# Performance work log

Hardware: AMD Instinct MI355X
Metric: run time of the kernel (lower is better)

## Reference

```python
import jax, jax.numpy as jnp
import numpy as np

PS, PAD, STRIDE = 3, 1, 1  # patch_size, padding, strides


def _unfold(x, ps, pad, stride):
    # torch F.unfold: [N, C, H, W] -> [N, C*ps*ps, L], channel-major (c, i, j) ordering
    N, C, H, Wd = x.shape
    xp = jnp.pad(x, ((0, 0), (0, 0), (pad, pad), (pad, pad)))
    Ho = (H + 2 * pad - ps) // stride + 1
    Wo = (Wd + 2 * pad - ps) // stride + 1
    cols = [xp[:, :, i:i + stride * Ho:stride, j:j + stride * Wo:stride]
            for i in range(ps) for j in range(ps)]  # ps*ps tensors of [N, C, Ho, Wo]
    cols = jnp.stack(cols, axis=2)                  # [N, C, ps*ps, Ho, Wo]
    return cols.reshape(N, C * ps * ps, Ho * Wo)


def _fold(cols, out_hw, ps, pad, stride):
    # torch F.fold (scatter-add inverse of unfold)
    N, CPP, L = cols.shape
    C = CPP // (ps * ps)
    H, Wd = out_hw
    Ho = (H + 2 * pad - ps) // stride + 1
    Wo = (Wd + 2 * pad - ps) // stride + 1
    cols = cols.reshape(N, C, ps, ps, Ho, Wo)
    out = jnp.zeros((N, C, H + 2 * pad, Wd + 2 * pad), cols.dtype)
    for i in range(ps):
        for j in range(ps):
            out = out.at[:, :, i:i + stride * Ho:stride, j:j + stride * Wo:stride].add(cols[:, :, i, j])
    return out[:, :, pad:pad + H, pad:pad + Wd]


def _l2norm(x, eps=1e-12):
    n = jnp.sqrt(jnp.sum(x * x, axis=-1, keepdims=True))
    return x / jnp.maximum(n, eps)


def setup_inputs() -> dict:
    key = jax.random.key(0)
    k1, k2, k3, k4 = jax.random.split(key, 4)
    shp = (2, 64, 5, 5, 48, 48)  # b, c, ah, aw, h, w
    return {
        "x1": jax.random.normal(k1, shp, dtype=jnp.float32),
        "x2": jax.random.normal(k2, shp, dtype=jnp.float32),
        "x3": jax.random.normal(k3, shp, dtype=jnp.float32),
        "W": jax.random.normal(k4, (8, 64), dtype=jnp.float32) * 0.05,  # 1x1 conv, c -> c//8
    }


def reference(x1, x2, x3, W):
    b, c, ah, aw, h, w = x1.shape
    A = ah * aw

    def flat(x):  # b c ah aw h w -> (b ah aw) c h w
        return x.transpose(0, 2, 3, 1, 4, 5).reshape(b * A, c, h, w)

    q = jnp.einsum('oc,nchw->nohw', W, flat(x1))  # 1x1 conv, no bias
    k = jnp.einsum('oc,nchw->nohw', W, flat(x2))
    v = flat(x3)

    qc = _unfold(q, PS, PAD, STRIDE)  # [(b ah aw), p_q, L]
    kc = _unfold(k, PS, PAD, STRIDE)
    vc = _unfold(v, PS, PAD, STRIDE)  # [(b ah aw), p_v, L]
    L = vc.shape[-1]
    p_v = vc.shape[1]

    def re(t):  # (b ah aw) p n -> b n (ah aw p)
        p = t.shape[1]
        return t.reshape(b, A, p, L).transpose(0, 3, 1, 2).reshape(b, L, A * p)

    Q = _l2norm(re(qc))
    K = _l2norm(re(kc))
    V = re(vc)  # [b, L, A*p_v]

    attn = jnp.einsum('bnd,bmd->bnm', Q, K)       # [b, L, L] cosine similarity
    idx = jnp.argmax(attn, axis=-1)               # [b, L] hard attention
    out = jnp.take_along_axis(V, idx[:, :, None], axis=1)  # gather rows of V

    # b n (ah aw p) -> (b ah aw) p n
    out = out.reshape(b, L, A, p_v).transpose(0, 2, 3, 1).reshape(b * A, p_v, L)
    out = _fold(out, (h, w), PS, PAD, STRIDE)     # [(b ah aw), c, h, w]
    return out.reshape(b, ah, aw, c, h, w).transpose(0, 3, 1, 2, 4, 5)
```

## Files before the change

### kernel.cpp

```cpp
#include <hip/hip_runtime.h>
#include <math.h>
#include <float.h>

#define NPIX 2304
#define NPAD 2500
#define PLANE 573440
#define MARGIN 3e-4f

#define OFF_QP     0u
#define OFF_KP     1146880u
#define OFF_PLANES 2293760u
#define OFF_NK     4587520u
#define OFF_INVNK  4592520u
#define OFF_PVAL   4597128u
#define OFF_PSEC   4818312u
#define OFF_PIDX   5039496u
#define OFF_IDX    5260680u
#define OFF_S      5269896u
#define OFF_SOFF   OFF_S
#define SSTRIDE    6250000L
#define PLANE_SH   573440

typedef __attribute__((ext_vector_type(8))) short short8;
typedef __attribute__((ext_vector_type(4))) float f32x4;

__device__ __forceinline__ unsigned short bfhi(float f) {
    unsigned u = __float_as_uint(f);
    return (unsigned short)((u + 0x7FFFu + ((u >> 16) & 1u)) >> 16);
}

__device__ __forceinline__ void gload_lds16(const void* g, void* l) {
    __builtin_amdgcn_global_load_lds(
        (const __attribute__((address_space(1))) unsigned int*)g,
        (__attribute__((address_space(3))) unsigned int*)l, 16, 0, 0);
}

__global__ __launch_bounds__(256) void k_zero(float4* __restrict__ p, int n4) {
    int i = blockIdx.x * 256 + threadIdx.x;
    const int stride = gridDim.x * 256;
    const float4 z = { 0.f, 0.f, 0.f, 0.f };
    for (; i < n4; i += stride) p[i] = z;
}

__global__ __launch_bounds__(256) void k_qk(const float* __restrict__ x1,
                                            const float* __restrict__ x2,
                                            const float* __restrict__ W,
                                            float* __restrict__ qp,
                                            float* __restrict__ kp,
                                            unsigned short* __restrict__ planes) {
    __shared__ float Ws[512];
    const int t = threadIdx.x;
    Ws[t] = W[t];
    Ws[t + 256] = W[t + 256];
    __syncthreads();
    const int img = blockIdx.x / 9;
    const int chunk = blockIdx.x % 9;
    const int pix = chunk * 256 + t;
    const int b = img / 25, a = img % 25;
    const int y = pix / 48, x = pix % 48;

    float q[8], k[8];
#pragma unroll
    for (int o = 0; o < 8; ++o) { q[o] = 0.f; k[o] = 0.f; }

    const float* p1 = x1 + (size_t)b * 64 * 57600 + a * 2304 + pix;
    const float* p2 = x2 + (size_t)b * 64 * 57600 + a * 2304 + pix;
#pragma unroll 8
    for (int c = 0; c < 64; ++c) {
        float v1 = p1[c * 57600];
        float v2 = p2[c * 57600];
#pragma unroll
        for (int o = 0; o < 8; ++o) {
            float w = Ws[o * 64 + c];
            q[o] = fmaf(w, v1, q[o]);
            k[o] = fmaf(w, v2, k[o]);
        }
    }
    const int p = (y + 1) * 50 + (x + 1);
    float* qd = qp + (size_t)b * PLANE + (size_t)p * 224 + a * 8;
    float* kd = kp + (size_t)b * PLANE + (size_t)p * 224 + a * 8;
    float4 q0 = { q[0], q[1], q[2], q[3] }, q1 = { q[4], q[5], q[6], q[7] };
    float4 k0 = { k[0], k[1], k[2], k[3] }, k1 = { k[4], k[5], k[6], k[7] };
    *(float4*)qd = q0; *(float4*)(qd + 4) = q1;
    *(float4*)kd = k0; *(float4*)(kd + 4) = k1;

    const int P = p >> 7, r = p & 127, cc = a >> 2, dq = a & 3;
    const int g = r * 4 + ((dq + (r >> 1)) & 3);
    const size_t goff = ((size_t)(P * 7 + cc) * 512 + g) * 8;
    short8 qh, ql, kh, kl;
#pragma unroll
    for (int o = 0; o < 8; ++o) {
        unsigned short h = bfhi(q[o]);
        qh[o] = (short)h;
        ql[o] = (short)bfhi(q[o] - __uint_as_float(((unsigned)h) << 16));
        h = bfhi(k[o]);
        kh[o] = (short)h;
        kl[o] = (short)bfhi(k[o] - __uint_as_float(((unsigned)h) << 16));
    }
    *(short8*)(planes + (size_t)(0 * 2 + b) * PLANE_SH + goff) = qh;
    *(short8*)(planes + (size_t)(1 * 2 + b) * PLANE_SH + goff) = ql;
    *(short8*)(planes + (size_t)(2 * 2 + b) * PLANE_SH + goff) = kh;
    *(short8*)(planes + (size_t)(3 * 2 + b) * PLANE_SH + goff) = kl;
}

__global__ void k_nk(const float* __restrict__ kp, float* __restrict__ nk) {
    int t = blockIdx.x * 256 + threadIdx.x;
    if (t >= 2 * NPAD) return;
    int b = t / NPAD, p = t - b * NPAD;
    const float* src = kp + (size_t)b * PLANE + (size_t)p * 224;
    float s = 0.f;
    for (int d = 0; d < 200; d += 4) {
        float4 v = *(const float4*)(src + d);
        s = fmaf(v.x, v.x, s); s = fmaf(v.y, v.y, s);
        s = fmaf(v.z, v.z, s); s = fmaf(v.w, v.w, s);
    }
    nk[t] = s;
}

__global__ void k_invnk(const float* __restrict__ nk, float* __restrict__ invNk) {
    int t = blockIdx.x * 256 + threadIdx.x;
    if (t >= 2 * NPIX) return;
    int b = t / NPIX, m = t - b * NPIX;
    int my = m / 48, mx = m % 48;
    const float* nb = nk + b * NPAD;
    float s = 0.f;
#pragma unroll
    for (int i = 0; i < 3; ++i)
#pragma unroll
        for (int j = 0; j < 3; ++j)
            s += nb[(my + i) * 50 + mx + j];
    invNk[t] = 1.0f / fmaxf(sqrtf(s), 1e-12f);
}

__global__ __launch_bounds__(256, 2) void k_mfma2(const unsigned short* __restrict__ planes,
                                                  float* __restrict__ S,
                                                  long sStride, int bofs) {
    __shared__ unsigned short Abuf[2][4096];
    __shared__ unsigned short Bbuf[2][4096];
    const int t = threadIdx.x;
    const int nwg = gridDim.x * gridDim.y * gridDim.z;
    const int lin = (blockIdx.z * gridDim.y + blockIdx.y) * gridDim.x + blockIdx.x;
    const int work = (lin & 7) * (nwg >> 3) + (lin >> 3);
    const int z = work / 400;
    const int rem = work - z * 400;
    const int wy = rem / 20, wx = rem - (rem / 20) * 20;
    const int b = bofs + z;

    const unsigned short* Ahi = planes + (size_t)(0 * 2 + b) * PLANE_SH;
    const unsigned short* Alo = planes + (size_t)(1 * 2 + b) * PLANE_SH;
    const unsigned short* Bhi = planes + (size_t)(2 * 2 + b) * PLANE_SH;
    const unsigned short* Blo = planes + (size_t)(3 * 2 + b) * PLANE_SH;
    float* Sb = S + (size_t)z * sStride;

    const int p0 = wy * 128, r0 = wx * 128;
    const int wid = t >> 6, l = t & 63;
    const int lp = l & 15, dq = l >> 4;
    const int wqp = (wid >> 1) * 64, wqr = (wid & 1) * 64;

    int aoff[4], boff[4];
#pragma unroll
    for (int tr = 0; tr < 4; ++tr) {
        int rA = wqp + tr * 16 + lp;
        aoff[tr] = (rA * 4 + ((dq + (rA >> 1)) & 3)) * 8;
        int rB = wqr + tr * 16 + lp;
        boff[tr] = (rB * 4 + ((dq + (rB >> 1)) & 3)) * 8;
    }

    f32x4 acc[4][4];
#pragma unroll
    for (int i = 0; i < 4; ++i)
#pragma unroll
        for (int j = 0; j < 4; ++j) acc[i][j] = (f32x4){0.f, 0.f, 0.f, 0.f};

#define STAGE(buf, ks)                                                          \
    {                                                                           \
        const int term = (ks) / 7, c = (ks) - term * 7;                         \
        const unsigned short* gA = (term < 2 ? Ahi : Alo) + ((size_t)(wy * 7 + c) << 12); \
        const unsigned short* gB = (term != 1 ? Bhi : Blo) + ((size_t)(wx * 7 + c) << 12); \
        unsigned short* lA = &Abuf[buf][wid * 512];                             \
        unsigned short* lB = &Bbuf[buf][wid * 512];                             \
        gload_lds16(gA + t * 8, lA);                                            \
        gload_lds16(gA + 2048 + t * 8, lA + 2048);                              \
        gload_lds16(gB + t * 8, lB);                                            \
        gload_lds16(gB + 2048 + t * 8, lB + 2048);                              \
    }

    STAGE(0, 0);
    asm volatile("s_waitcnt vmcnt(0)" ::: "memory");
    __syncthreads();

    int cur = 0;
    for (int ks = 0; ks < 21; ++ks) {
        if (ks + 1 < 21) STAGE(cur ^ 1, ks + 1);
        {
            const unsigned short* Ab = &Abuf[cur][0];
            const unsigned short* Bb = &Bbuf[cur][0];
            short8 af[4], bfr[4];
#pragma unroll
            for (int tr = 0; tr < 4; ++tr) af[tr] = *(const short8*)(Ab + aoff[tr]);
#pragma unroll
            for (int tc = 0; tc < 4; ++tc) bfr[tc] = *(const short8*)(Bb + boff[tc]);
#pragma unroll
            for (int tr = 0; tr < 4; ++tr)
#pragma unroll
                for (int tc = 0; tc < 4; ++tc)
                    acc[tr][tc] = __builtin_amdgcn_mfma_f32_16x16x32_bf16(
                        af[tr], bfr[tc], acc[tr][tc], 0, 0, 0);
        }
        if (ks + 1 < 21) {
            asm volatile("s_waitcnt vmcnt(0)" ::: "memory");
            __syncthreads();
            cur ^= 1;
        }
    }
#undef STAGE

#pragma unroll
    for (int tr = 0; tr < 4; ++tr) {
#pragma unroll
        for (int v = 0; v < 4; ++v) {
            const int p = p0 + wqp + tr * 16 + dq * 4 + v;
            if (p < NPAD) {
                float* srow_ = Sb + (size_t)p * NPAD;
#pragma unroll
                for (int tc = 0; tc < 4; ++tc) {
                    const int c = r0 + wqr + tc * 16 + lp;
                    if (c < NPAD) srow_[c] = acc[tr][tc][v];
                }
            }
        }
    }
}

__global__ __launch_bounds__(384) void k_argmax(const float* __restrict__ S,
                                                const float* __restrict__ invNk,
                                                float* __restrict__ pval,
                                                float* __restrict__ psec,
                                                int* __restrict__ pidx,
                                                long sStride, int bofs) {
    __shared__ float band[3][50][50];
    const int t = threadIdx.x;
    const int nwg = gridDim.x * gridDim.y * gridDim.z;
    const int lin = (blockIdx.z * gridDim.y + blockIdx.y) * gridDim.x + blockIdx.x;
    const int work = (lin & 7) * (nwg >> 3) + (lin >> 3);
    const int z = work / 2304;
    const int w2 = work - z * 2304;
    const int ly = w2 / 48;
    const int my = w2 - ly * 48;
    const int batch = bofs + z;
    const float* Sb = S + (size_t)z * sStride;

    {
        const int rt = t >> 3, ct = t & 7;
        for (int rr = rt; rr < 150; rr += 48) {
            const int i = (rr >= 100) ? 2 : (rr >= 50 ? 1 : 0);
            const int uu = rr - i * 50;
            const float* srow = Sb + (size_t)((ly + i) * 50 + uu) * NPAD + (my + i) * 50;
            float* drow = &band[i][uu][0];
            *(float2*)(drow + 2 * ct)      = *(const float2*)(srow + 2 * ct);
            *(float2*)(drow + 16 + 2 * ct) = *(const float2*)(srow + 16 + 2 * ct);
            *(float2*)(drow + 32 + 2 * ct) = *(const float2*)(srow + 32 + 2 * ct);
            if (ct == 0) *(float2*)(drow + 48) = *(const float2*)(srow + 48);
        }
    }
    __syncthreads();

    const int lx = t >> 3;
    const int mc = t & 7;
    const float* inb = invNk + batch * NPIX;
    const float* bp = &band[0][lx][mc];

    float b1 = -FLT_MAX, b2 = -FLT_MAX;
    int i1 = 0x7FFFFFFF;

#pragma unroll
    for (int k = 0; k < 6; ++k) {
        const float* p = bp + 8 * k;
        float s = p[0]    + p[51]   + p[102]
                + p[2500] + p[2551] + p[2602]
                + p[5000] + p[5051] + p[5102];
        int m = my * 48 + mc + (k << 3);
        float v = s * inb[m];
        if (v > b1 || (v == b1 && m < i1)) { b2 = b1; b1 = v; i1 = m; }
        else b2 = fmaxf(b2, v);
    }
#pragma unroll
    for (int off = 1; off < 8; off <<= 1) {
        float ob1 = __shfl_xor(b1, off, 64);
        int oi1 = __shfl_xor(i1, off, 64);
        float ob2 = __shfl_xor(b2, off, 64);
        if (ob1 > b1 || (ob1 == b1 && oi1 < i1)) { b2 = fmaxf(b1, ob2); b1 = ob1; i1 = oi1; }
        else b2 = fmaxf(b2, ob1);
    }
    if (mc == 0) {
        int o = (batch * 48 + my) * NPIX + ly * 48 + lx;
        pval[o] = b1;
        psec[o] = b2;
        pidx[o] = i1;
    }
}

__global__ __launch_bounds__(256) void k_sel(const float* __restrict__ qp,
                                             const float* __restrict__ kp,
                                             const float* __restrict__ S,
                                             const float* __restrict__ invNk,
                                             const float* __restrict__ pval,
                                             const float* __restrict__ psec,
                                             const int* __restrict__ pidx,
                                             int* __restrict__ idx,
                                             long sStride, int bofs) {
    const int t = threadIdx.x;
    const int lane = t & 63;
    const int row = blockIdx.x * 4 + (t >> 6);
    const int z = blockIdx.y;
    const int b = bofs + z;

    float v1 = -FLT_MAX, v2 = -FLT_MAX;
    int ii = 0x7FFFFFFF;
    if (lane < 48) {
        int o = (b * 48 + lane) * NPIX + row;
        v1 = pval[o];
        v2 = psec[o];
        ii = pidx[o];
    }
    float r1 = v1, r2 = v2;
    int ri = ii;
#pragma unroll
    for (int off = 1; off < 64; off <<= 1) {
        float o1 = __shfl_xor(r1, off, 64);
        int oi = __shfl_xor(ri, off, 64);
        float o2 = __shfl_xor(r2, off, 64);
        if (o1 > r1 || (o1 == r1 && oi < ri)) { r2 = fmaxf(o2, r1); r1 = o1; ri = oi; }
        else r2 = fmaxf(r2, o1);
    }
    if (lane == 0) idx[b * NPIX + row] = ri;
    if (r1 - r2 >= MARGIN) return;

    const float* Sb = S + (size_t)z * sStride;
    const float* Ap = qp + (size_t)b * PLANE;
    const float* Bp = kp + (size_t)b * PLANE;
    const float* inb = invNk + b * NPIX;
    const int ly = row / 48, lx = row % 48;
    const float th = r1 - MARGIN;

    unsigned long long mask = __ballot(lane < 48 && (v1 >= th || v2 >= th));
    float eb = -FLT_MAX;
    int ebi = 0x7FFFFFFF;
    while (mask) {
        const int my = __ffsll((long long)mask) - 1;
        mask &= mask - 1;
        float va = -FLT_MAX;
        if (lane < 48) {
            float s = 0.f;
#pragma unroll
            for (int i = 0; i < 3; ++i)
#pragma unroll
                for (int j = 0; j < 3; ++j)
                    s += Sb[(size_t)((ly + i) * 50 + lx + j) * NPAD + (my + i) * 50 + lane + j];
            va = s * inb[my * 48 + lane];
        }
        unsigned long long m2 = __ballot(lane < 48 && va >= th);
        while (m2) {
            const int mx = __ffsll((long long)m2) - 1;
            m2 &= m2 - 1;
            const int m = my * 48 + mx;
            float part = 0.f;
#pragma unroll
            for (int ij = 0; ij < 9; ++ij) {
                const float* qr = Ap + (size_t)((ly + ij / 3) * 50 + lx + ij % 3) * 224;
                const float* kr = Bp + (size_t)((my + ij / 3) * 50 + mx + ij % 3) * 224;
                for (int d = lane; d < 200; d += 64)
                    part = fmaf(qr[d], kr[d], part);
            }
#pragma unroll
            for (int off = 1; off < 64; off <<= 1)
                part += __shfl_xor(part, off, 64);
            const float v = part * inb[m];
            if (v > eb) { eb = v; ebi = m; }
        }
    }
    if (lane == 0 && ebi != 0x7FFFFFFF) idx[b * NPIX + row] = ebi;
}

__global__ void k_soff(const int* __restrict__ idx, int* __restrict__ soff) {
    int t = blockIdx.x * 256 + threadIdx.x;
    if (t >= 2 * NPIX) return;
    int b = t / NPIX, pix = t - b * NPIX;
    int y = pix / 48, x = pix % 48;
#pragma unroll
    for (int i = 0; i < 3; ++i) {
#pragma unroll
        for (int j = 0; j < 3; ++j) {
            int u = i * 3 + j;
            int yq = y + 1 - i, xq = x + 1 - j;
            int so = -1;
            if (yq >= 0 && yq < 48 && xq >= 0 && xq < 48) {
                int m = idx[b * NPIX + yq * 48 + xq];
                int my = m / 48, mx = m % 48;
                int yy = my + i - 1, xx = mx + j - 1;
                if (yy >= 0 && yy < 48 && xx >= 0 && xx < 48) so = yy * 48 + xx;
            }
            soff[(b * 9 + u) * NPIX + pix] = so;
        }
    }
}

#define CPB 4
__global__ __launch_bounds__(256) void k_out2(const float* __restrict__ x3,
                                              const int* __restrict__ soff,
                                              float* __restrict__ out) {
    __shared__ __align__(16) float plane[NPIX];
    const int t = threadIdx.x;
    const int img = blockIdx.x;
    const int b = img / 25, a = img % 25;

    int po[9][9];
#pragma unroll
    for (int u = 0; u < 9; ++u) {
        const int* sb = soff + (b * 9 + u) * NPIX;
#pragma unroll
        for (int k = 0; k < 9; ++k)
            po[k][u] = sb[k * 256 + t];
    }

    const size_t pbase = (size_t)b * 64 * 57600 + (size_t)a * 2304 +
                         (size_t)(blockIdx.y * CPB) * 57600;
    const float* gsrc = x3 + pbase;
    float* gdst = out + pbase;

    float4 r0, r1, r2;
    {
        const float4* g = (const float4*)gsrc;
        r0 = g[t]; r1 = g[t + 256];
        if (t < 64) r2 = g[t + 512];
    }
    float4* pl4 = (float4*)plane;
    pl4[t] = r0; pl4[t + 256] = r1;
    if (t < 64) pl4[t + 512] = r2;
    __syncthreads();

    for (int c = 0; c < CPB; ++c) {
        if (c + 1 < CPB) {
            const float4* g = (const float4*)(gsrc + (size_t)(c + 1) * 57600);
            r0 = g[t]; r1 = g[t + 256];
            if (t < 64) r2 = g[t + 512];
        }
        float* dst = gdst + (size_t)c * 57600;
#pragma unroll
        for (int k = 0; k < 9; ++k) {
            float acc = 0.f;
#pragma unroll
            for (int u = 0; u < 9; ++u) {
                int off = po[k][u];
                int ao = off < 0 ? 0 : off;
                float v = plane[ao];
                acc += (off < 0) ? 0.f : v;
            }
            dst[k * 256 + t] = acc;
        }
        __syncthreads();
        if (c + 1 < CPB) {
            pl4[t] = r0; pl4[t + 256] = r1;
            if (t < 64) pl4[t + 512] = r2;
        }
        __syncthreads();
    }
}

extern "C" void kernel_launch(void* const* d_in, const int* in_sizes, int n_in,
                              void* d_out, int out_size, void* d_ws, size_t ws_size,
                              hipStream_t stream) {
    const float* x1 = (const float*)d_in[0];
    const float* x2 = (const float*)d_in[1];
    const float* x3 = (const float*)d_in[2];
    const float* W  = (const float*)d_in[3];
    float* ws = (float*)d_ws;

    float* qp    = ws + OFF_QP;
    float* kp    = ws + OFF_KP;
    unsigned short* planes = (unsigned short*)(ws + OFF_PLANES);
    float* nk    = ws + OFF_NK;
    float* invNk = ws + OFF_INVNK;
    float* pval  = ws + OFF_PVAL;
    float* psec  = ws + OFF_PSEC;
    int*   pidx  = (int*)(ws + OFF_PIDX);
    int*   idx   = (int*)(ws + OFF_IDX);
    float* S     = ws + OFF_S;
    int*   soff  = (int*)(ws + OFF_SOFF);
    float* out   = (float*)d_out;

    const bool bigS = ws_size >= (size_t)(OFF_S + 2UL * (unsigned long)SSTRIDE) * 4UL;

    k_zero<<<2048, 256, 0, stream>>>((float4*)(ws + OFF_QP), (int)(OFF_NK / 4));

    k_qk<<<450, 256, 0, stream>>>(x1, x2, W, qp, kp, planes);
    k_nk<<<(2 * NPAD + 255) / 256, 256, 0, stream>>>(kp, nk);
    k_invnk<<<(2 * NPIX + 255) / 256, 256, 0, stream>>>(nk, invNk);

    if (bigS) {
        k_mfma2<<<dim3(20, 20, 2), 256, 0, stream>>>(planes, S, SSTRIDE, 0);
        k_argmax<<<dim3(48, 48, 2), 384, 0, stream>>>(S, invNk, pval, psec, pidx, SSTRIDE, 0);
        k_sel<<<dim3(576, 2), 256, 0, stream>>>(qp, kp, S, invNk, pval, psec, pidx,
                                                idx, SSTRIDE, 0);
    } else {
        for (int b = 0; b < 2; ++b) {
            k_mfma2<<<dim3(20, 20, 1), 256, 0, stream>>>(planes, S, 0L, b);
            k_argmax<<<dim3(48, 48, 1), 384, 0, stream>>>(S, invNk, pval, psec, pidx, 0L, b);
            k_sel<<<dim3(576, 1), 256, 0, stream>>>(qp, kp, S, invNk, pval, psec, pidx,
                                                    idx, 0L, b);
        }
    }
    k_soff<<<(2 * NPIX + 255) / 256, 256, 0, stream>>>(idx, soff);
    k_out2<<<dim3(50, 16), 256, 0, stream>>>(x3, soff, out);
}
```

Measured before the change: 147.5 us.

## Pack last K-chunk of split-bf16 GEMM terms into one shared tail stage

The split-precision GEMM used three passes (hi*hi, hi*lo, lo*hi) over 7 K-chunks each, where the 7th chunk holds only one angular position. This change builds a separate tail plane in which that last chunk's three term products are laid side by side, one per 8-wide group, with the fourth group zeroed. All three terms are then covered in a single extra stage, cutting the MFMA loop from 21 to 19 stages. It also merges the key-norm and 3x3 window-sum kernels into one, which drops a launch but recomputes each patch norm up to nine times.

```diff
diff --git a/kernel.cpp b/kernel.cpp
--- a/kernel.cpp
+++ b/kernel.cpp
@@ -10,13 +10,13 @@
 #define OFF_QP     0u
 #define OFF_KP     1146880u
 #define OFF_PLANES 2293760u
-#define OFF_NK     4587520u
-#define OFF_INVNK  4592520u
-#define OFF_PVAL   4597128u
-#define OFF_PSEC   4818312u
-#define OFF_PIDX   5039496u
-#define OFF_IDX    5260680u
-#define OFF_S      5269896u
+#define OFF_TAIL   4587520u
+#define OFF_INVNK  4751360u
+#define OFF_PVAL   4755968u
+#define OFF_PSEC   4977152u
+#define OFF_PIDX   5198336u
+#define OFF_IDX    5419520u
+#define OFF_S      5424128u
 #define OFF_SOFF   OFF_S
 #define SSTRIDE    6250000L
 #define PLANE_SH   573440
@@ -47,7 +47,8 @@
                                             const float* __restrict__ W,
                                             float* __restrict__ qp,
                                             float* __restrict__ kp,
-                                            unsigned short* __restrict__ planes) {
+                                            unsigned short* __restrict__ planes,
+                                            unsigned short* __restrict__ tail) {
     __shared__ float Ws[512];
     const int t = threadIdx.x;
     Ws[t] = W[t];
@@ -101,38 +102,50 @@
     *(short8*)(planes + (size_t)(1 * 2 + b) * PLANE_SH + goff) = ql;
     *(short8*)(planes + (size_t)(2 * 2 + b) * PLANE_SH + goff) = kh;
     *(short8*)(planes + (size_t)(3 * 2 + b) * PLANE_SH + goff) = kl;
-}
-
-__global__ void k_nk(const float* __restrict__ kp, float* __restrict__ nk) {
-    int t = blockIdx.x * 256 + threadIdx.x;
-    if (t >= 2 * NPAD) return;
-    int b = t / NPAD, p = t - b * NPAD;
-    const float* src = kp + (size_t)b * PLANE + (size_t)p * 224;
-    float s = 0.f;
-    for (int d = 0; d < 200; d += 4) {
-        float4 v = *(const float4*)(src + d);
-        s = fmaf(v.x, v.x, s); s = fmaf(v.y, v.y, s);
-        s = fmaf(v.z, v.z, s); s = fmaf(v.w, v.w, s);
-    }
-    nk[t] = s;
-}
-
-__global__ void k_invnk(const float* __restrict__ nk, float* __restrict__ invNk) {
+
+    if (a == 24) {
+        unsigned short* qt = tail + (((size_t)(0 * 2 + b) * 20 + P) << 12);
+        unsigned short* kt = tail + (((size_t)(1 * 2 + b) * 20 + P) << 12);
+        short8 zz = { 0, 0, 0, 0, 0, 0, 0, 0 };
+#define GOF(qq) ((r * 4 + (((qq) + (r >> 1)) & 3)) * 8)
+        *(short8*)(qt + GOF(0)) = qh;
+        *(short8*)(qt + GOF(1)) = qh;
+        *(short8*)(qt + GOF(2)) = ql;
+        *(short8*)(qt + GOF(3)) = zz;
+        *(short8*)(kt + GOF(0)) = kh;
+        *(short8*)(kt + GOF(1)) = kl;
+        *(short8*)(kt + GOF(2)) = kh;
+        *(short8*)(kt + GOF(3)) = zz;
+#undef GOF
+    }
+}
+
+__global__ void k_norm(const float* __restrict__ kp, float* __restrict__ invNk) {
     int t = blockIdx.x * 256 + threadIdx.x;
     if (t >= 2 * NPIX) return;
     int b = t / NPIX, m = t - b * NPIX;
     int my = m / 48, mx = m % 48;
-    const float* nb = nk + b * NPAD;
     float s = 0.f;
 #pragma unroll
-    for (int i = 0; i < 3; ++i)
-#pragma unroll
-        for (int j = 0; j < 3; ++j)
-            s += nb[(my + i) * 50 + mx + j];
+    for (int i = 0; i < 3; ++i) {
+#pragma unroll
+        for (int j = 0; j < 3; ++j) {
+            const int p = (my + i) * 50 + mx + j;
+            const float* src = kp + (size_t)b * PLANE + (size_t)p * 224;
+            float sp = 0.f;
+            for (int d = 0; d < 200; d += 4) {
+                float4 v = *(const float4*)(src + d);
+                sp = fmaf(v.x, v.x, sp); sp = fmaf(v.y, v.y, sp);
+                sp = fmaf(v.z, v.z, sp); sp = fmaf(v.w, v.w, sp);
+            }
+            s += sp;
+        }
+    }
     invNk[t] = 1.0f / fmaxf(sqrtf(s), 1e-12f);
 }
 
 __global__ __launch_bounds__(256, 2) void k_mfma2(const unsigned short* __restrict__ planes,
+                                                  const unsigned short* __restrict__ tail,
                                                   float* __restrict__ S,
                                                   long sStride, int bofs) {
     __shared__ unsigned short Abuf[2][4096];
@@ -174,9 +187,15 @@
 
 #define STAGE(buf, ks)                                                          \
     {                                                                           \
-        const int term = (ks) / 7, c = (ks) - term * 7;                         \
-        const unsigned short* gA = (term < 2 ? Ahi : Alo) + ((size_t)(wy * 7 + c) << 12); \
-        const unsigned short* gB = (term != 1 ? Bhi : Blo) + ((size_t)(wx * 7 + c) << 12); \
+        const unsigned short *gA, *gB;                                          \
+        if ((ks) < 18) {                                                        \
+            const int term = (ks) / 6, c = (ks) - term * 6;                     \
+            gA = (term < 2 ? Ahi : Alo) + ((size_t)(wy * 7 + c) << 12);         \
+            gB = (term != 1 ? Bhi : Blo) + ((size_t)(wx * 7 + c) << 12);        \
+        } else {                                                                \
+            gA = tail + (((size_t)(0 * 2 + b) * 20 + wy) << 12);                \
+            gB = tail + (((size_t)(1 * 2 + b) * 20 + wx) << 12);                \
+        }                                                                       \
         unsigned short* lA = &Abuf[buf][wid * 512];                             \
         unsigned short* lB = &Bbuf[buf][wid * 512];                             \
         gload_lds16(gA + t * 8, lA);                                            \
@@ -190,8 +209,8 @@
     __syncthreads();
 
     int cur = 0;
-    for (int ks = 0; ks < 21; ++ks) {
-        if (ks + 1 < 21) STAGE(cur ^ 1, ks + 1);
+    for (int ks = 0; ks < 19; ++ks) {
+        if (ks + 1 < 19) STAGE(cur ^ 1, ks + 1);
         {
             const unsigned short* Ab = &Abuf[cur][0];
             const unsigned short* Bb = &Bbuf[cur][0];
@@ -207,7 +226,7 @@
                     acc[tr][tc] = __builtin_amdgcn_mfma_f32_16x16x32_bf16(
                         af[tr], bfr[tc], acc[tr][tc], 0, 0, 0);
         }
-        if (ks + 1 < 21) {
+        if (ks + 1 < 19) {
             asm volatile("s_waitcnt vmcnt(0)" ::: "memory");
             __syncthreads();
             cur ^= 1;
@@ -479,7 +498,7 @@
     float* qp    = ws + OFF_QP;
     float* kp    = ws + OFF_KP;
     unsigned short* planes = (unsigned short*)(ws + OFF_PLANES);
-    float* nk    = ws + OFF_NK;
+    unsigned short* tail   = (unsigned short*)(ws + OFF_TAIL);
     float* invNk = ws + OFF_INVNK;
     float* pval  = ws + OFF_PVAL;
     float* psec  = ws + OFF_PSEC;
@@ -491,20 +510,19 @@
 
     const bool bigS = ws_size >= (size_t)(OFF_S + 2UL * (unsigned long)SSTRIDE) * 4UL;
 
-    k_zero<<<2048, 256, 0, stream>>>((float4*)(ws + OFF_QP), (int)(OFF_NK / 4));
-
-    k_qk<<<450, 256, 0, stream>>>(x1, x2, W, qp, kp, planes);
-    k_nk<<<(2 * NPAD + 255) / 256, 256, 0, stream>>>(kp, nk);
-    k_invnk<<<(2 * NPIX + 255) / 256, 256, 0, stream>>>(nk, invNk);
+    k_zero<<<2048, 256, 0, stream>>>((float4*)(ws + OFF_QP), (int)(OFF_INVNK / 4));
+
+    k_qk<<<450, 256, 0, stream>>>(x1, x2, W, qp, kp, planes, tail);
+    k_norm<<<(2 * NPIX + 255) / 256, 256, 0, stream>>>(kp, invNk);
 
     if (bigS) {
-        k_mfma2<<<dim3(20, 20, 2), 256, 0, stream>>>(planes, S, SSTRIDE, 0);
+        k_mfma2<<<dim3(20, 20, 2), 256, 0, stream>>>(planes, tail, S, SSTRIDE, 0);
         k_argmax<<<dim3(48, 48, 2), 384, 0, stream>>>(S, invNk, pval, psec, pidx, SSTRIDE, 0);
         k_sel<<<dim3(576, 2), 256, 0, stream>>>(qp, kp, S, invNk, pval, psec, pidx,
                                                 idx, SSTRIDE, 0);
     } else {
         for (int b = 0; b < 2; ++b) {
-            k_mfma2<<<dim3(20, 20, 1), 256, 0, stream>>>(planes, S, 0L, b);
+            k_mfma2<<<dim3(20, 20, 1), 256, 0, stream>>>(planes, tail, S, 0L, b);
             k_argmax<<<dim3(48, 48, 1), 384, 0, stream>>>(S, invNk, pval, psec, pidx, 0L, b);
             k_sel<<<dim3(576, 1), 256, 0, stream>>>(qp, kp, S, invNk, pval, psec, pidx,
                                                     idx, 0L, b);
```

Measured after the change: 197.3 us. 33.8% more time.
